# Performance work log

Hardware: AMD Instinct MI355X
Metric: run time of the kernel (lower is better)

## Reference

```python
import jax, jax.numpy as jnp
import numpy as np

L, B, S, D, H, F = 4, 2, 2048, 768, 12, 3072
HD = D // H
EPS = 1e-5


def _ln(x, g, b):
    m = jnp.mean(x, axis=-1, keepdims=True)
    v = jnp.mean((x - m) ** 2, axis=-1, keepdims=True)
    return (x - m) * jax.lax.rsqrt(v + EPS) * g + b


def setup_inputs() -> dict:
    key = jax.random.key(0)
    ks = jax.random.split(key, 12)
    s = 0.02
    n = lambda k, shp: jax.random.normal(k, shp, jnp.float32) * s
    return {
        "inputs": jax.random.normal(ks[0], (B, S, D), jnp.float32),
        "attn_mask": jax.random.randint(ks[1], (B, S, S), 0, 2) == 1,
        "Wq": n(ks[2], (L, D, D)), "bq": jnp.zeros((L, D), jnp.float32),
        "Wk": n(ks[3], (L, D, D)), "bk": jnp.zeros((L, D), jnp.float32),
        "Wv": n(ks[4], (L, D, D)), "bv": jnp.zeros((L, D), jnp.float32),
        "Wo": n(ks[5], (L, D, D)), "bo": jnp.zeros((L, D), jnp.float32),
        "ln1_g": jnp.ones((L, D), jnp.float32), "ln1_b": jnp.zeros((L, D), jnp.float32),
        "W1": n(ks[6], (L, F, D)), "b1": jnp.zeros((L, F), jnp.float32),
        "W2": n(ks[7], (L, D, F)), "b2": jnp.zeros((L, D), jnp.float32),
        "ln2_g": jnp.ones((L, D), jnp.float32), "ln2_b": jnp.zeros((L, D), jnp.float32),
    }


def reference(inputs, attn_mask, Wq, bq, Wk, bk, Wv, bv, Wo, bo,
              ln1_g, ln1_b, W1, b1, W2, b2, ln2_g, ln2_b):
    x = inputs
    scale = 1.0 / (HD ** 0.5)
    mask = attn_mask[:, None, :, :]  # [B,1,S,S] broadcasts over heads
    nlayers = Wq.shape[0]
    for i in range(nlayers):
        # torch Linear: y = x @ W.T + b, W stored [out,in]
        q = (jnp.einsum('bsd,ed->bse', x, Wq[i]) + bq[i]).reshape(B, S, H, HD)
        k = (jnp.einsum('bsd,ed->bse', x, Wk[i]) + bk[i]).reshape(B, S, H, HD)
        v = (jnp.einsum('bsd,ed->bse', x, Wv[i]) + bv[i]).reshape(B, S, H, HD)
        scores = jnp.einsum('bqhd,bkhd->bhqk', q, k) * scale
        scores = jnp.where(mask, jnp.float32(-1e9), scores)
        p = jax.nn.softmax(scores, axis=-1)
        ctx = jnp.einsum('bhqk,bkhd->bqhd', p, v).reshape(B, S, D)
        attn = jnp.einsum('bsd,ed->bse', ctx, Wo[i]) + bo[i]
        x = _ln(attn + x, ln1_g[i], ln1_b[i])
        h = jax.nn.relu(jnp.einsum('bsd,fd->bsf', x, W1[i]) + b1[i])
        ff = jnp.einsum('bsf,df->bsd', h, W2[i]) + b2[i]
        x = _ln(ff + x, ln2_g[i], ln2_b[i])
    return x
```

## Files before the change

kernel.cpp:

```cpp
#include <hip/hip_runtime.h>
#include <cmath>
#include <cstdint>
#include <cstddef>


typedef __bf16 bf16_t;
typedef __bf16 bf16x8 __attribute__((ext_vector_type(8)));
typedef __bf16 bf16x4 __attribute__((ext_vector_type(4)));
typedef float  f32x4  __attribute__((ext_vector_type(4)));
typedef float  f32x16 __attribute__((ext_vector_type(16)));
typedef int    i32x2  __attribute__((ext_vector_type(2)));

#define DEV static __device__ __forceinline__

constexpr int Lc = 4, Bc = 2, Sc = 2048, Dc = 768, Hc = 12, Fc = 3072, HDc = 64;
constexpr int Mrows = Bc * Sc;
#define QSCALE 0.18033688011112042f

DEV f32x4 mfma16(bf16x8 a, bf16x8 b, f32x4 c) {
  return __builtin_amdgcn_mfma_f32_16x16x32_bf16(a, b, c, 0, 0, 0);
}
DEV f32x16 mfma32(bf16x8 a, bf16x8 b, f32x16 c) {
  return __builtin_amdgcn_mfma_f32_32x32x16_bf16(a, b, c, 0, 0, 0);
}

DEV void gload_lds16(const void* g, void* l) {
  __builtin_amdgcn_global_load_lds(
      (const __attribute__((address_space(1))) void*)g,
      (__attribute__((address_space(3))) void*)l,
      16, 0, 0);
}

DEV float fexp2(float x) { return __builtin_amdgcn_exp2f(x); }

DEV unsigned cvtpk(float lo, float hi_) {
  unsigned r;
  asm("v_cvt_pk_bf16_f32 %0, %1, %2" : "=v"(r) : "v"(lo), "v"(hi_));
  return r;
}
DEV void swapl(unsigned &a, unsigned &b) {
  i32x2 r = __builtin_amdgcn_permlane32_swap((int)a, (int)b, false, false);
  a = (unsigned)r[0];
  b = (unsigned)r[1];
}
DEV bf16x8 frag4(unsigned a, unsigned b, unsigned c, unsigned d) {
  union { unsigned u[4]; bf16x8 v; } x;
  x.u[0] = a; x.u[1] = b; x.u[2] = c; x.u[3] = d;
  return x.v;
}


__global__ __launch_bounds__(256) void cvt_weights_kernel(
    const float* __restrict__ Wq, const float* __restrict__ Wk,
    const float* __restrict__ Wv, const float* __restrict__ Wo,
    const float* __restrict__ W1, const float* __restrict__ W2,
    bf16_t* __restrict__ wqkv, bf16_t* __restrict__ wo,
    bf16_t* __restrict__ w1, bf16_t* __restrict__ w2) {
  constexpr int DD = Dc * Dc;
  constexpr int nDD = Lc * DD;
  constexpr int nFD = Lc * Fc * Dc;
  int i = (blockIdx.x * 256 + threadIdx.x) * 4;
  const float* src;
  bf16_t* dst;
  if (i < 3 * nDD) {
    int sub = i / nDD, r = i - sub * nDD;
    int l = r / DD, off = r - l * DD;
    src = (sub == 0 ? Wq : (sub == 1 ? Wk : Wv)) + r;
    dst = wqkv + (size_t)(l * 3 + sub) * DD + off;
  } else if (i < 4 * nDD) {
    int r = i - 3 * nDD;
    src = Wo + r; dst = wo + r;
  } else if (i < 4 * nDD + nFD) {
    int r = i - 4 * nDD;
    src = W1 + r; dst = w1 + r;
  } else {
    int r = i - 4 * nDD - nFD;
    src = W2 + r; dst = w2 + r;
  }
  float4 v = *(const float4*)src;
  bf16x4 o;
  o[0] = (bf16_t)v.x; o[1] = (bf16_t)v.y; o[2] = (bf16_t)v.z; o[3] = (bf16_t)v.w;
  *(bf16x4*)dst = o;
}

__global__ __launch_bounds__(256) void init_x_kernel(const float* __restrict__ in,
                                                     float* __restrict__ x,
                                                     bf16_t* __restrict__ xb, int n) {
  int i = (blockIdx.x * 256 + threadIdx.x) * 4;
  if (i + 3 < n) {
    float4 v = *(const float4*)(in + i);
    *(float4*)(x + i) = v;
    bf16x4 o;
    o[0] = (bf16_t)v.x; o[1] = (bf16_t)v.y; o[2] = (bf16_t)v.z; o[3] = (bf16_t)v.w;
    *(bf16x4*)(xb + i) = o;
  }
}

__global__ __launch_bounds__(256) void mask_packT_kernel(const int* __restrict__ m,
                                                         unsigned long long* __restrict__ bits) {
  size_t gid = (size_t)blockIdx.x * 256 + threadIdx.x;
  int l = (int)(gid & 63);
  size_t widx = gid >> 6;
  size_t q = widx & (Sc - 1);
  size_t bkw = widx >> 11;
  size_t kw = bkw & (Sc / 64 - 1);
  size_t b = bkw >> 5;
  unsigned long long bm = __ballot(m[(b * Sc + q) * Sc + kw * 64 + l] != 0);
  if (l == 0) bits[widx] = bm;
}

__global__ __launch_bounds__(256) void gemm_ffn1(const bf16_t* __restrict__ A,
                                                 const bf16_t* __restrict__ Bm,
                                                 const float* __restrict__ bias,
                                                 bf16_t* __restrict__ Cb,
                                                 int M, int N, int K) {
  __shared__ bf16_t sA[2 * 64 * 64];
  __shared__ bf16_t sB[2 * 128 * 64];
  const int tid = threadIdx.x;
  const int w = tid >> 6, l = tid & 63, lg = l >> 4, li = l & 15;
  const int wr = w >> 1, wc = w & 1;
  const int nwg = gridDim.x, cpx = nwg >> 3;
  const int id = blockIdx.x;
  const int tid2 = (id & 7) * cpx + (id >> 3);
  const int nbx = M / 64;
  const int tm = (tid2 % nbx) * 64, tn = (tid2 / nbx) * 128;
  const int nk = K >> 6;

  f32x4 acc[2][4];
#pragma unroll
  for (int m = 0; m < 2; m++)
#pragma unroll
    for (int n = 0; n < 4; n++) acc[m][n] = (f32x4){0.f, 0.f, 0.f, 0.f};

  auto stage = [&](int buf, int kt) {
    const int k0 = kt * 64;
#pragma unroll
    for (int i = 0; i < 2; i++) {
      int off = i * 2048 + tid * 8;
      gload_lds16(A + (size_t)(tm + (off >> 6)) * K + k0 + (off & 63),
                  &sA[buf * 4096 + i * 2048 + w * 512]);
    }
#pragma unroll
    for (int i = 0; i < 4; i++) {
      int off = i * 2048 + tid * 8;
      gload_lds16(Bm + (size_t)(tn + (off >> 6)) * K + k0 + (off & 63),
                  &sB[buf * 8192 + i * 2048 + w * 512]);
    }
  };

  stage(0, 0);
  asm volatile("s_waitcnt vmcnt(0)" ::: "memory");
  __builtin_amdgcn_s_barrier();
  asm volatile("" ::: "memory");
  int cur = 0;
  for (int kt = 0; kt < nk; kt++) {
    if (kt + 1 < nk) stage(cur ^ 1, kt + 1);
    const bf16_t* sAb = &sA[cur * 4096];
    const bf16_t* sBb = &sB[cur * 8192];
#pragma unroll
    for (int kk = 0; kk < 2; kk++) {
      bf16x8 af[2], bfr[4];
#pragma unroll
      for (int m = 0; m < 2; m++)
        af[m] = *(const bf16x8*)&sAb[(wr * 32 + m * 16 + li) * 64 + kk * 32 + lg * 8];
#pragma unroll
      for (int n = 0; n < 4; n++)
        bfr[n] = *(const bf16x8*)&sBb[(wc * 64 + n * 16 + li) * 64 + kk * 32 + lg * 8];
#pragma unroll
      for (int m = 0; m < 2; m++)
#pragma unroll
        for (int n = 0; n < 4; n++)
          acc[m][n] = mfma16(af[m], bfr[n], acc[m][n]);
    }
    asm volatile("s_waitcnt vmcnt(0)" ::: "memory");
    __builtin_amdgcn_s_barrier();
    asm volatile("" ::: "memory");
    cur ^= 1;
  }

#pragma unroll
  for (int m = 0; m < 2; m++) {
    int rbase = tm + wr * 32 + m * 16 + lg * 4;
#pragma unroll
    for (int n = 0; n < 4; n++) {
      int c = tn + wc * 64 + n * 16 + li;
      float bv = bias[c];
#pragma unroll
      for (int j = 0; j < 4; j++)
        Cb[(size_t)(rbase + j) * N + c] = (bf16_t)fmaxf(acc[m][n][j] + bv, 0.f);
    }
  }
}

__global__ __launch_bounds__(256) void gemm_sk(const bf16_t* __restrict__ A,
                                               const bf16_t* __restrict__ Bm,
                                               float* __restrict__ P0,
                                               float* __restrict__ P1,
                                               int M, int N, int K) {
  __shared__ bf16_t sA[2 * 64 * 64];
  __shared__ bf16_t sB[2 * 128 * 64];
  const int tid = threadIdx.x;
  const int w = tid >> 6, l = tid & 63, lg = l >> 4, li = l & 15;
  const int wr = w >> 1, wc = w & 1;
  const int nwg = gridDim.x, cpx = nwg >> 3;
  const int id = blockIdx.x;
  const int tid2 = (id & 7) * cpx + (id >> 3);
  const int half = nwg >> 1;
  const int ks = tid2 >= half ? 1 : 0;
  const int r = tid2 - ks * half;
  const int nbx = M / 64;
  const int tm = (r % nbx) * 64, tn = (r / nbx) * 128;
  const int kB = K >> 1;
  const int k0base = ks * kB;
  const int nk = kB >> 6;
  float* __restrict__ P = ks ? P1 : P0;

  f32x4 acc[2][4];
#pragma unroll
  for (int m = 0; m < 2; m++)
#pragma unroll
    for (int n = 0; n < 4; n++) acc[m][n] = (f32x4){0.f, 0.f, 0.f, 0.f};

  auto stage = [&](int buf, int kt) {
    const int k0 = k0base + kt * 64;
#pragma unroll
    for (int i = 0; i < 2; i++) {
      int off = i * 2048 + tid * 8;
      gload_lds16(A + (size_t)(tm + (off >> 6)) * K + k0 + (off & 63),
                  &sA[buf * 4096 + i * 2048 + w * 512]);
    }
#pragma unroll
    for (int i = 0; i < 4; i++) {
      int off = i * 2048 + tid * 8;
      gload_lds16(Bm + (size_t)(tn + (off >> 6)) * K + k0 + (off & 63),
                  &sB[buf * 8192 + i * 2048 + w * 512]);
    }
  };

  stage(0, 0);
  asm volatile("s_waitcnt vmcnt(0)" ::: "memory");
  __builtin_amdgcn_s_barrier();
  asm volatile("" ::: "memory");
  int cur = 0;
  for (int kt = 0; kt < nk; kt++) {
    if (kt + 1 < nk) stage(cur ^ 1, kt + 1);
    const bf16_t* sAb = &sA[cur * 4096];
    const bf16_t* sBb = &sB[cur * 8192];
#pragma unroll
    for (int kk = 0; kk < 2; kk++) {
      bf16x8 af[2], bfr[4];
#pragma unroll
      for (int m = 0; m < 2; m++)
        af[m] = *(const bf16x8*)&sAb[(wr * 32 + m * 16 + li) * 64 + kk * 32 + lg * 8];
#pragma unroll
      for (int n = 0; n < 4; n++)
        bfr[n] = *(const bf16x8*)&sBb[(wc * 64 + n * 16 + li) * 64 + kk * 32 + lg * 8];
#pragma unroll
      for (int m = 0; m < 2; m++)
#pragma unroll
        for (int n = 0; n < 4; n++)
          acc[m][n] = mfma16(af[m], bfr[n], acc[m][n]);
    }
    asm volatile("s_waitcnt vmcnt(0)" ::: "memory");
    __builtin_amdgcn_s_barrier();
    asm volatile("" ::: "memory");
    cur ^= 1;
  }

#pragma unroll
  for (int m = 0; m < 2; m++) {
    int rbase = tm + wr * 32 + m * 16 + lg * 4;
#pragma unroll
    for (int n = 0; n < 4; n++) {
      int c = tn + wc * 64 + n * 16 + li;
#pragma unroll
      for (int j = 0; j < 4; j++)
        P[(size_t)(rbase + j) * N + c] = acc[m][n][j];
    }
  }
}

__global__ __launch_bounds__(256) void gemm_qkv(const bf16_t* __restrict__ A,
                                                const bf16_t* __restrict__ Bm,
                                                const float* __restrict__ bq,
                                                const float* __restrict__ bk,
                                                const float* __restrict__ bv,
                                                bf16_t* __restrict__ qo,
                                                bf16_t* __restrict__ ko,
                                                bf16_t* __restrict__ vTo) {
  constexpr int K = Dc;
  __shared__ bf16_t sA[2 * 64 * 64];
  __shared__ bf16_t sB[2 * 128 * 64];
  const int tid = threadIdx.x;
  const int w = tid >> 6, l = tid & 63, lg = l >> 4, li = l & 15;
  const int wr = w >> 1, wc = w & 1;
  const int nwg = gridDim.x, cpx = nwg >> 3;
  const int id = blockIdx.x;
  const int tid2 = (id & 7) * cpx + (id >> 3);
  constexpr int nbx = Mrows / 64;
  const int tm = (tid2 % nbx) * 64, tn = (tid2 / nbx) * 128;
  constexpr int nk = K >> 6;

  f32x4 acc[2][4];
#pragma unroll
  for (int m = 0; m < 2; m++)
#pragma unroll
    for (int n = 0; n < 4; n++) acc[m][n] = (f32x4){0.f, 0.f, 0.f, 0.f};

  auto stage = [&](int buf, int kt) {
    const int k0 = kt * 64;
#pragma unroll
    for (int i = 0; i < 2; i++) {
      int off = i * 2048 + tid * 8;
      gload_lds16(A + (size_t)(tm + (off >> 6)) * K + k0 + (off & 63),
                  &sA[buf * 4096 + i * 2048 + w * 512]);
    }
#pragma unroll
    for (int i = 0; i < 4; i++) {
      int off = i * 2048 + tid * 8;
      gload_lds16(Bm + (size_t)(tn + (off >> 6)) * K + k0 + (off & 63),
                  &sB[buf * 8192 + i * 2048 + w * 512]);
    }
  };

  stage(0, 0);
  asm volatile("s_waitcnt vmcnt(0)" ::: "memory");
  __builtin_amdgcn_s_barrier();
  asm volatile("" ::: "memory");
  int cur = 0;
  for (int kt = 0; kt < nk; kt++) {
    if (kt + 1 < nk) stage(cur ^ 1, kt + 1);
    const bf16_t* sAb = &sA[cur * 4096];
    const bf16_t* sBb = &sB[cur * 8192];
#pragma unroll
    for (int kk = 0; kk < 2; kk++) {
      bf16x8 af[2], bfr[4];
#pragma unroll
      for (int m = 0; m < 2; m++)
        af[m] = *(const bf16x8*)&sAb[(wr * 32 + m * 16 + li) * 64 + kk * 32 + lg * 8];
#pragma unroll
      for (int n = 0; n < 4; n++)
        bfr[n] = *(const bf16x8*)&sBb[(wc * 64 + n * 16 + li) * 64 + kk * 32 + lg * 8];
#pragma unroll
      for (int m = 0; m < 2; m++)
#pragma unroll
        for (int n = 0; n < 4; n++)
          acc[m][n] = mfma16(af[m], bfr[n], acc[m][n]);
    }
    asm volatile("s_waitcnt vmcnt(0)" ::: "memory");
    __builtin_amdgcn_s_barrier();
    asm volatile("" ::: "memory");
    cur ^= 1;
  }

  const int which = tn / 768;
#pragma unroll
  for (int m = 0; m < 2; m++) {
    int rbase = tm + wr * 32 + m * 16 + lg * 4;
#pragma unroll
    for (int n = 0; n < 4; n++) {
      int c = tn + wc * 64 + n * 16 + li;
      int col = c - which * 768;
      if (which == 0) {
        float bvv = bq[col];
#pragma unroll
        for (int j = 0; j < 4; j++)
          qo[(size_t)(rbase + j) * Dc + col] = (bf16_t)((acc[m][n][j] + bvv) * QSCALE);
      } else if (which == 1) {
        float bvv = bk[col];
#pragma unroll
        for (int j = 0; j < 4; j++)
          ko[(size_t)(rbase + j) * Dc + col] = (bf16_t)(acc[m][n][j] + bvv);
      } else {
        float bvv = bv[col];
        int h = col >> 6, d = col & 63;
        int b = rbase >> 11, s0 = rbase & 2047;
        bf16x4 pk;
#pragma unroll
        for (int j = 0; j < 4; j++) pk[j] = (bf16_t)(acc[m][n][j] + bvv);
        *(bf16x4*)(vTo + ((size_t)(b * Hc + h) * HDc + d) * Sc + s0) = pk;
      }
    }
  }
}

__global__ __launch_bounds__(256) void attn7_kernel(
    const bf16_t* __restrict__ q, const bf16_t* __restrict__ k,
    const bf16_t* __restrict__ vT, const unsigned long long* __restrict__ maskT,
    bf16_t* __restrict__ ctx) {
  __shared__ __align__(16) char smem[32768];

  const int t = threadIdx.x, w = t >> 6, l = t & 63;
  const int hi = l >> 5, li = l & 31;
  const int wp = w & 1, kvh = w >> 1;
  const int gid = blockIdx.x;
  const int tid2 = (gid & 7) * 96 + (gid >> 3);
  const int bh = tid2 >> 5, qt = tid2 & 31;
  const int b = bh / Hc, h = bh - b * Hc;
  const int qrow = qt * 64 + wp * 32 + li;

  const bf16_t* qp = q + (size_t)(b * Sc + qrow) * Dc + h * HDc + hi * 8;
  bf16x8 qf[4];
#pragma unroll
  for (int dk = 0; dk < 4; dk++) qf[dk] = *(const bf16x8*)(qp + dk * 16);

  const bf16_t* kg = k + ((size_t)(b * Sc) + kvh * 1024) * Dc + h * HDc;
  const bf16_t* vg = vT + (size_t)bh * HDc * Sc + kvh * 1024;
  const unsigned long long* mg =
      maskT + (size_t)b * 32 * Sc + (size_t)(kvh * 16) * Sc + qrow;

  f32x16 o0, o1;
#pragma unroll
  for (int r = 0; r < 16; r++) { o0[r] = 0.f; o1[r] = 0.f; }
  float ps = 0.f;

  auto stage = [&](int buf, int c) {
    const int kv0 = c * 32;
    bf16_t* sk = (bf16_t*)(smem + kvh * 16384 + buf * 8192);
    bf16_t* sv = (bf16_t*)(smem + kvh * 16384 + buf * 8192 + 4096);
#pragma unroll
    for (int i = 0; i < 2; i++) {
      int s = i * 128 + wp * 64 + l;
      int row = s >> 3, ch = s & 7;
      gload_lds16(kg + (size_t)(kv0 + row) * Dc + ((ch ^ (row & 7)) * 8),
                  sk + (i * 128 + wp * 64) * 8);
    }
#pragma unroll
    for (int i = 0; i < 2; i++) {
      int s = i * 128 + wp * 64 + l;
      int row = s >> 2, ch = s & 3;
      gload_lds16(vg + (size_t)row * Sc + kv0 + ((ch ^ ((row >> 1) & 3)) * 8),
                  sv + (i * 128 + wp * 64) * 8);
    }
  };

  stage(0, 0);
  __syncthreads();
  int cur = 0;
  unsigned long long mw = 0;
#pragma unroll 2
  for (int c = 0; c < 32; c++) {
    if (c + 1 < 32) stage(cur ^ 1, c + 1);
    if ((c & 1) == 0) mw = mg[(size_t)(c >> 1) * Sc];
    unsigned msel = (c & 1) ? (unsigned)(mw >> 32) : (unsigned)mw;
    unsigned ms0 = msel >> (hi * 4);

    f32x16 sc0;
#pragma unroll
    for (int r = 0; r < 16; r++) sc0[r] = 0.f;
    const bf16_t* kb = (const bf16_t*)(smem + kvh * 16384 + cur * 8192);
    __builtin_amdgcn_s_setprio(1);
#pragma unroll
    for (int dk = 0; dk < 4; dk++) {
      int ch = dk * 2 + hi;
      bf16x8 ka0 = *(const bf16x8*)(kb + li * 64 + ((ch ^ (li & 7)) * 8));
      sc0 = mfma32(ka0, qf[dk], sc0);
    }
    __builtin_amdgcn_s_setprio(0);

    unsigned pw[8];
#pragma unroll
    for (int r = 0; r < 16; r += 2) {
      int kbit = (r & 3) + 8 * (r >> 2);
      float a0 = fexp2(sc0[r]), a1 = fexp2(sc0[r + 1]);
      a0 = ((ms0 >> kbit) & 1u) ? 0.f : a0;
      a1 = ((ms0 >> (kbit + 1)) & 1u) ? 0.f : a1;
      ps += a0 + a1;
      pw[r >> 1] = cvtpk(a0, a1);
    }
    swapl(pw[0], pw[2]);  swapl(pw[1], pw[3]);
    swapl(pw[4], pw[6]);  swapl(pw[5], pw[7]);
    bf16x8 pb0 = frag4(pw[0], pw[1], pw[2], pw[3]);
    bf16x8 pb1 = frag4(pw[4], pw[5], pw[6], pw[7]);

    const bf16_t* vb = (const bf16_t*)(smem + kvh * 16384 + cur * 8192 + 4096);
    __builtin_amdgcn_s_setprio(1);
#pragma unroll
    for (int g = 0; g < 2; g++) {
      int ch = g * 2 + hi;
      bf16x8 va0 = *(const bf16x8*)(vb + li * 32 + ((ch ^ ((li >> 1) & 3)) * 8));
      bf16x8 va1 = *(const bf16x8*)(vb + (32 + li) * 32 + ((ch ^ ((li >> 1) & 3)) * 8));
      bf16x8 pbg = (g == 0) ? pb0 : pb1;
      o0 = mfma32(va0, pbg, o0);
      o1 = mfma32(va1, pbg, o1);
    }
    __builtin_amdgcn_s_setprio(0);
    __syncthreads();
    cur ^= 1;
  }

  float* mp = (float*)(smem + 16384);
  if (kvh == 1) {
    char* base = smem + wp * 8192 + l * 128;
#pragma unroll
    for (int r = 0; r < 4; r++) {
      *(f32x4*)(base + ((r ^ (l & 7)) * 16)) =
          (f32x4){o0[r * 4], o0[r * 4 + 1], o0[r * 4 + 2], o0[r * 4 + 3]};
      *(f32x4*)(base + (((r + 4) ^ (l & 7)) * 16)) =
          (f32x4){o1[r * 4], o1[r * 4 + 1], o1[r * 4 + 2], o1[r * 4 + 3]};
    }
    mp[wp * 64 + l] = ps;
  }
  __syncthreads();
  float inv = 0.f;
  if (kvh == 0) {
    char* base = smem + wp * 8192 + l * 128;
#pragma unroll
    for (int r = 0; r < 4; r++) {
      f32x4 u = *(const f32x4*)(base + ((r ^ (l & 7)) * 16));
      f32x4 v = *(const f32x4*)(base + (((r + 4) ^ (l & 7)) * 16));
#pragma unroll
      for (int j = 0; j < 4; j++) { o0[r * 4 + j] += u[j]; o1[r * 4 + j] += v[j]; }
    }
    ps += mp[wp * 64 + l];
    float tot = ps + __shfl_xor(ps, 32, 64);
    inv = 1.f / tot;
  }
  __syncthreads();
  if (kvh == 0) {
    char* so = smem + wp * 4096;
    const int lx = li & 7;
#pragma unroll
    for (int g = 0; g < 4; g++) {
      unsigned u0 = cvtpk(o0[g * 4 + 0] * inv, o0[g * 4 + 1] * inv);
      unsigned u1 = cvtpk(o0[g * 4 + 2] * inv, o0[g * 4 + 3] * inv);
      unsigned v0 = cvtpk(o1[g * 4 + 0] * inv, o1[g * 4 + 1] * inv);
      unsigned v1 = cvtpk(o1[g * 4 + 2] * inv, o1[g * 4 + 3] * inv);
      *(uint2*)(so + li * 128 + ((g ^ lx) * 16) + hi * 8) = make_uint2(u0, u1);
      *(uint2*)(so + li * 128 + (((g + 4) ^ lx) * 16) + hi * 8) = make_uint2(v0, v1);
    }
    __builtin_amdgcn_s_waitcnt(0);
    bf16_t* cbase = ctx + (size_t)(b * Sc + qt * 64 + wp * 32) * Dc + h * HDc;
#pragma unroll
    for (int i = 0; i < 4; i++) {
      int s = i * 64 + l;
      int row = s >> 3, ch = s & 7;
      bf16x8 vv = *(const bf16x8*)(so + row * 128 + ((ch ^ (row & 7)) * 16));
      *(bf16x8*)(cbase + (size_t)row * Dc + ch * 8) = vv;
    }
  }
}

__global__ __launch_bounds__(256) void ln_fuse_kernel(const float* __restrict__ p0,
                                                      const float* __restrict__ p1,
                                                      const float* __restrict__ bias,
                                                      const float* res,
                                                      const float* __restrict__ g,
                                                      const float* __restrict__ bb,
                                                      float* xo, bf16_t* __restrict__ xb) {
  const int row = blockIdx.x;
  const int t = threadIdx.x;
  const size_t base = (size_t)row * Dc;
  float v0 = p0[base + t] + p1[base + t] + bias[t] + res[base + t];
  float v1 = p0[base + t + 256] + p1[base + t + 256] + bias[t + 256] + res[base + t + 256];
  float v2 = p0[base + t + 512] + p1[base + t + 512] + bias[t + 512] + res[base + t + 512];
  float s = v0 + v1 + v2;
  float sq = v0 * v0 + v1 * v1 + v2 * v2;
#pragma unroll
  for (int ofs = 1; ofs < 64; ofs <<= 1) {
    s += __shfl_xor(s, ofs, 64);
    sq += __shfl_xor(sq, ofs, 64);
  }
  __shared__ float red[8];
  const int w = t >> 6, l = t & 63;
  if (l == 0) { red[w] = s; red[4 + w] = sq; }
  __syncthreads();
  s = red[0] + red[1] + red[2] + red[3];
  sq = red[4] + red[5] + red[6] + red[7];
  const float mean = s * (1.f / Dc);
  const float var = sq * (1.f / Dc) - mean * mean;
  const float rs = rsqrtf(var + 1e-5f);
  float* po = xo + base;
  bf16_t* pb = xb + base;
#pragma unroll
  for (int i = 0; i < 3; i++) {
    int d = t + i * 256;
    float vv = (i == 0 ? v0 : (i == 1 ? v1 : v2));
    float ov = (vv - mean) * rs * g[d] + bb[d];
    po[d] = ov;
    pb[d] = (bf16_t)ov;
  }
}


extern "C" void kernel_launch(void* const* d_in, const int* in_sizes, int n_in,
                              void* d_out, int out_size, void* d_ws, size_t ws_size,
                              hipStream_t stream) {
  const float* inputs = (const float*)d_in[0];
  const int* amask = (const int*)d_in[1];
  const float* Wq = (const float*)d_in[2];
  const float* bq = (const float*)d_in[3];
  const float* Wk = (const float*)d_in[4];
  const float* bk = (const float*)d_in[5];
  const float* Wv = (const float*)d_in[6];
  const float* bv = (const float*)d_in[7];
  const float* Wo = (const float*)d_in[8];
  const float* bo = (const float*)d_in[9];
  const float* ln1_g = (const float*)d_in[10];
  const float* ln1_b = (const float*)d_in[11];
  const float* W1 = (const float*)d_in[12];
  const float* b1 = (const float*)d_in[13];
  const float* W2 = (const float*)d_in[14];
  const float* b2 = (const float*)d_in[15];
  const float* ln2_g = (const float*)d_in[16];
  const float* ln2_b = (const float*)d_in[17];
  float* xout = (float*)d_out;

  char* p = (char*)d_ws;
  auto carve = [&](size_t bytes) -> char* {
    char* r = p;
    p += (bytes + 255) & ~(size_t)255;
    return r;
  };
  const size_t nDD = (size_t)Lc * Dc * Dc;
  const size_t nFD = (size_t)Lc * Fc * Dc;
  const size_t nAct = (size_t)Mrows * Dc;
  const size_t nHid = (size_t)Mrows * Fc;

  bf16_t* wqkv16 = (bf16_t*)carve(nDD * 3 * 2);
  bf16_t* wo16 = (bf16_t*)carve(nDD * 2);
  bf16_t* w1_16 = (bf16_t*)carve(nFD * 2);
  bf16_t* w2_16 = (bf16_t*)carve(nFD * 2);
  bf16_t* xb = (bf16_t*)carve(nAct * 2);
  bf16_t* q16 = (bf16_t*)carve(nAct * 2);
  bf16_t* k16 = (bf16_t*)carve(nAct * 2);
  bf16_t* vTb = (bf16_t*)carve(nAct * 2);
  bf16_t* ctx = (bf16_t*)carve(nAct * 2);
  bf16_t* h16 = (bf16_t*)carve(nHid * 2);
  float* attnf = (float*)carve(nAct * 4);
  float* ff = (float*)carve(nAct * 4);
  unsigned long long* maskb = (unsigned long long*)carve((size_t)Bc * (Sc / 64) * Sc * 8);
  (void)ws_size; (void)n_in; (void)in_sizes; (void)out_size;

  dim3 blk(256);

  mask_packT_kernel<<<(int)((size_t)Bc * Sc * Sc / 256), blk, 0, stream>>>(amask, maskb);
  cvt_weights_kernel<<<(int)((4 * nDD + 2 * nFD) / 1024), blk, 0, stream>>>(
      Wq, Wk, Wv, Wo, W1, W2, wqkv16, wo16, w1_16, w2_16);
  init_x_kernel<<<(int)(nAct / 1024), blk, 0, stream>>>(inputs, xout, xb, (int)nAct);

  for (int i = 0; i < Lc; i++) {
    const bf16_t* wqkv_l = wqkv16 + (size_t)i * 3 * Dc * Dc;
    const bf16_t* wo_l = wo16 + (size_t)i * Dc * Dc;
    const bf16_t* w1_l = w1_16 + (size_t)i * Fc * Dc;
    const bf16_t* w2_l = w2_16 + (size_t)i * Dc * Fc;

    gemm_qkv<<<1152, blk, 0, stream>>>(
        xb, wqkv_l, bq + (size_t)i * Dc, bk + (size_t)i * Dc, bv + (size_t)i * Dc,
        q16, k16, vTb);

    attn7_kernel<<<768, blk, 0, stream>>>(q16, k16, vTb, maskb, ctx);

    gemm_sk<<<768, blk, 0, stream>>>(ctx, wo_l, attnf, ff, Mrows, Dc, Dc);
    ln_fuse_kernel<<<Mrows, blk, 0, stream>>>(attnf, ff, bo + (size_t)i * Dc, xout,
                                              ln1_g + (size_t)i * Dc,
                                              ln1_b + (size_t)i * Dc, xout, xb);
    gemm_ffn1<<<1536, blk, 0, stream>>>(
        xb, w1_l, b1 + (size_t)i * Fc, h16, Mrows, Fc, Dc);
    gemm_sk<<<768, blk, 0, stream>>>(h16, w2_l, attnf, ff, Mrows, Dc, Fc);
    ln_fuse_kernel<<<Mrows, blk, 0, stream>>>(attnf, ff, b2 + (size_t)i * Dc, xout,
                                              ln2_g + (size_t)i * Dc,
                                              ln2_b + (size_t)i * Dc, xout, xb);
  }
}
```

Before: 800.7 us.

## Use partial vmcnt waits in GEMMs and triple-buffer attention K/V loads

In the three GEMM kernels, the loop now waits only for the current tile's loads (vmcnt(6)) before a barrier at the top of each iteration. This lets the next tile's global-to-LDS loads stay in flight during the MFMA work instead of draining them at the end of the iteration. The attention kernel moves to three K/V LDS buffers, with 48KB of shared memory and the loop manually unrolled by two. It prefetches the mask word one step ahead and uses counted vmcnt waits, so loads overlap compute with a single barrier per step. The extra LDS may reduce occupancy, and the hand-counted vmcnt values must exactly match the number of loads issued per stage.

```diff
diff --git a/kernel.cpp b/kernel.cpp
--- a/kernel.cpp
+++ b/kernel.cpp
@@ -48,6 +48,9 @@
   x.u[0] = a; x.u[1] = b; x.u[2] = c; x.u[3] = d;
   return x.v;
 }
+
+#define WAITV(N) asm volatile("s_waitcnt vmcnt(" #N ")" ::: "memory")
+#define BARRIER() do { __builtin_amdgcn_s_barrier(); asm volatile("" ::: "memory"); } while (0)
 
 
 __global__ __launch_bounds__(256) void cvt_weights_kernel(
@@ -149,12 +152,17 @@
   };
 
   stage(0, 0);
-  asm volatile("s_waitcnt vmcnt(0)" ::: "memory");
-  __builtin_amdgcn_s_barrier();
-  asm volatile("" ::: "memory");
+  WAITV(0);
+  BARRIER();
   int cur = 0;
   for (int kt = 0; kt < nk; kt++) {
-    if (kt + 1 < nk) stage(cur ^ 1, kt + 1);
+    if (kt + 1 < nk) {
+      stage(cur ^ 1, kt + 1);
+      WAITV(6);
+    } else {
+      WAITV(0);
+    }
+    BARRIER();
     const bf16_t* sAb = &sA[cur * 4096];
     const bf16_t* sBb = &sB[cur * 8192];
 #pragma unroll
@@ -172,9 +180,7 @@
         for (int n = 0; n < 4; n++)
           acc[m][n] = mfma16(af[m], bfr[n], acc[m][n]);
     }
-    asm volatile("s_waitcnt vmcnt(0)" ::: "memory");
-    __builtin_amdgcn_s_barrier();
-    asm volatile("" ::: "memory");
+    BARRIER();
     cur ^= 1;
   }
 
@@ -238,12 +244,17 @@
   };
 
   stage(0, 0);
-  asm volatile("s_waitcnt vmcnt(0)" ::: "memory");
-  __builtin_amdgcn_s_barrier();
-  asm volatile("" ::: "memory");
+  WAITV(0);
+  BARRIER();
   int cur = 0;
   for (int kt = 0; kt < nk; kt++) {
-    if (kt + 1 < nk) stage(cur ^ 1, kt + 1);
+    if (kt + 1 < nk) {
+      stage(cur ^ 1, kt + 1);
+      WAITV(6);
+    } else {
+      WAITV(0);
+    }
+    BARRIER();
     const bf16_t* sAb = &sA[cur * 4096];
     const bf16_t* sBb = &sB[cur * 8192];
 #pragma unroll
@@ -261,9 +272,7 @@
         for (int n = 0; n < 4; n++)
           acc[m][n] = mfma16(af[m], bfr[n], acc[m][n]);
     }
-    asm volatile("s_waitcnt vmcnt(0)" ::: "memory");
-    __builtin_amdgcn_s_barrier();
-    asm volatile("" ::: "memory");
+    BARRIER();
     cur ^= 1;
   }
 
@@ -324,12 +333,17 @@
   };
 
   stage(0, 0);
-  asm volatile("s_waitcnt vmcnt(0)" ::: "memory");
-  __builtin_amdgcn_s_barrier();
-  asm volatile("" ::: "memory");
+  WAITV(0);
+  BARRIER();
   int cur = 0;
   for (int kt = 0; kt < nk; kt++) {
-    if (kt + 1 < nk) stage(cur ^ 1, kt + 1);
+    if (kt + 1 < nk) {
+      stage(cur ^ 1, kt + 1);
+      WAITV(6);
+    } else {
+      WAITV(0);
+    }
+    BARRIER();
     const bf16_t* sAb = &sA[cur * 4096];
     const bf16_t* sBb = &sB[cur * 8192];
 #pragma unroll
@@ -347,9 +361,7 @@
         for (int n = 0; n < 4; n++)
           acc[m][n] = mfma16(af[m], bfr[n], acc[m][n]);
     }
-    asm volatile("s_waitcnt vmcnt(0)" ::: "memory");
-    __builtin_amdgcn_s_barrier();
-    asm volatile("" ::: "memory");
+    BARRIER();
     cur ^= 1;
   }
 
@@ -384,11 +396,11 @@
   }
 }
 
-__global__ __launch_bounds__(256) void attn7_kernel(
+__global__ __launch_bounds__(256) void attn8_kernel(
     const bf16_t* __restrict__ q, const bf16_t* __restrict__ k,
     const bf16_t* __restrict__ vT, const unsigned long long* __restrict__ maskT,
     bf16_t* __restrict__ ctx) {
-  __shared__ __align__(16) char smem[32768];
+  __shared__ __align__(16) char smem[49152];
 
   const int t = threadIdx.x, w = t >> 6, l = t & 63;
   const int hi = l >> 5, li = l & 31;
@@ -399,25 +411,27 @@
   const int b = bh / Hc, h = bh - b * Hc;
   const int qrow = qt * 64 + wp * 32 + li;
 
-  const bf16_t* qp = q + (size_t)(b * Sc + qrow) * Dc + h * HDc + hi * 8;
-  bf16x8 qf[4];
-#pragma unroll
-  for (int dk = 0; dk < 4; dk++) qf[dk] = *(const bf16x8*)(qp + dk * 16);
-
   const bf16_t* kg = k + ((size_t)(b * Sc) + kvh * 1024) * Dc + h * HDc;
   const bf16_t* vg = vT + (size_t)bh * HDc * Sc + kvh * 1024;
   const unsigned long long* mg =
       maskT + (size_t)b * 32 * Sc + (size_t)(kvh * 16) * Sc + qrow;
 
+  unsigned long long mwc = mg[0], mwn = 0;
+  const bf16_t* qp = q + (size_t)(b * Sc + qrow) * Dc + h * HDc + hi * 8;
+  bf16x8 qf[4];
+#pragma unroll
+  for (int dk = 0; dk < 4; dk++) qf[dk] = *(const bf16x8*)(qp + dk * 16);
+
   f32x16 o0, o1;
 #pragma unroll
   for (int r = 0; r < 16; r++) { o0[r] = 0.f; o1[r] = 0.f; }
   float ps = 0.f;
 
-  auto stage = [&](int buf, int c) {
+  auto stage = [&](int bno, int c) {
     const int kv0 = c * 32;
-    bf16_t* sk = (bf16_t*)(smem + kvh * 16384 + buf * 8192);
-    bf16_t* sv = (bf16_t*)(smem + kvh * 16384 + buf * 8192 + 4096);
+    char* base = smem + kvh * 24576 + bno * 8192;
+    bf16_t* sk = (bf16_t*)base;
+    bf16_t* sv = (bf16_t*)(base + 4096);
 #pragma unroll
     for (int i = 0; i < 2; i++) {
       int s = i * 128 + wp * 64 + l;
@@ -434,21 +448,12 @@
     }
   };
 
-  stage(0, 0);
-  __syncthreads();
-  int cur = 0;
-  unsigned long long mw = 0;
-#pragma unroll 2
-  for (int c = 0; c < 32; c++) {
-    if (c + 1 < 32) stage(cur ^ 1, c + 1);
-    if ((c & 1) == 0) mw = mg[(size_t)(c >> 1) * Sc];
-    unsigned msel = (c & 1) ? (unsigned)(mw >> 32) : (unsigned)mw;
+  auto computeT = [&](int bno, unsigned msel) {
     unsigned ms0 = msel >> (hi * 4);
-
     f32x16 sc0;
 #pragma unroll
     for (int r = 0; r < 16; r++) sc0[r] = 0.f;
-    const bf16_t* kb = (const bf16_t*)(smem + kvh * 16384 + cur * 8192);
+    const bf16_t* kb = (const bf16_t*)(smem + kvh * 24576 + bno * 8192);
     __builtin_amdgcn_s_setprio(1);
 #pragma unroll
     for (int dk = 0; dk < 4; dk++) {
@@ -473,7 +478,7 @@
     bf16x8 pb0 = frag4(pw[0], pw[1], pw[2], pw[3]);
     bf16x8 pb1 = frag4(pw[4], pw[5], pw[6], pw[7]);
 
-    const bf16_t* vb = (const bf16_t*)(smem + kvh * 16384 + cur * 8192 + 4096);
+    const bf16_t* vb = (const bf16_t*)(smem + kvh * 24576 + bno * 8192 + 4096);
     __builtin_amdgcn_s_setprio(1);
 #pragma unroll
     for (int g = 0; g < 2; g++) {
@@ -485,9 +490,38 @@
       o1 = mfma32(va1, pbg, o1);
     }
     __builtin_amdgcn_s_setprio(0);
-    __syncthreads();
-    cur ^= 1;
-  }
+  };
+
+  stage(0, 0);
+  WAITV(0);
+  BARRIER();
+  int bcur = 0;
+  for (int cp = 0; cp < 16; cp++) {
+    {
+      int bst = bcur == 2 ? 0 : bcur + 1;
+      if (cp < 15) mwn = mg[(size_t)(cp + 1) * Sc];
+      stage(bst, 2 * cp + 1);
+      if (cp < 15) WAITV(5); else WAITV(4);
+      BARRIER();
+      computeT(bcur, (unsigned)mwc);
+      bcur = bst;
+    }
+    {
+      int bst = bcur == 2 ? 0 : bcur + 1;
+      if (cp < 15) {
+        stage(bst, 2 * cp + 2);
+        WAITV(4);
+      } else {
+        WAITV(0);
+      }
+      BARRIER();
+      computeT(bcur, (unsigned)(mwc >> 32));
+      bcur = bst;
+      if (cp < 15) mwc = mwn;
+    }
+  }
+
+  __syncthreads();
 
   float* mp = (float*)(smem + 16384);
   if (kvh == 1) {
@@ -649,7 +683,7 @@
         xb, wqkv_l, bq + (size_t)i * Dc, bk + (size_t)i * Dc, bv + (size_t)i * Dc,
         q16, k16, vTb);
 
-    attn7_kernel<<<768, blk, 0, stream>>>(q16, k16, vTb, maskb, ctx);
+    attn8_kernel<<<768, blk, 0, stream>>>(q16, k16, vTb, maskb, ctx);
 
     gemm_sk<<<768, blk, 0, stream>>>(ctx, wo_l, attnf, ff, Mrows, Dc, Dc);
     ln_fuse_kernel<<<Mrows, blk, 0, stream>>>(attnf, ff, bo + (size_t)i * Dc, xout,
```

New measurement: 838.6 us. 4.7% more time.
